# Optimization experiments

Hardware: AMD Instinct MI355X
Metric: run time of the kernel (lower is better)

The kernel has to match this reference:

```python
import jax, jax.numpy as jnp
import numpy as np

EPS = 1e-6


def setup_inputs() -> dict:
    key = jax.random.key(0)
    k1, k2 = jax.random.split(key)
    B, K, N, d = 4, 16, 2048, 256
    return {
        "img_f": jax.random.normal(k1, (B, K, d), dtype=jnp.float32),
        "text_f": jax.random.normal(k2, (N, K, d), dtype=jnp.float32),
        "r": jnp.zeros((4,), dtype=jnp.float32),
        "alp": jnp.array([0.5], dtype=jnp.float32),
        "scale": jnp.array([1.0], dtype=jnp.float32),
        "logits_scales": jnp.array([0.5], dtype=jnp.float32),
    }


def _rc_dist_ItoT(I, T, alpha, beta):
    # I: (B,K,d) images, T: (N,K,d) texts -> dist (B,N)
    B, K, d = I.shape
    lam = (B / d) * jnp.exp(alpha) + EPS
    rho = jnp.exp(beta)
    ItI = jnp.einsum('bkd,bke->bde', I, I)                      # (B,d,d)
    Minv = jnp.linalg.inv(ItI + lam * jnp.eye(d, dtype=I.dtype))
    A = jnp.einsum('bde,bke->bdk', Minv, I)                      # (B,d,K) = Minv @ I^T
    # T_bar[b,n] = I[b] @ A[b] @ T[n]; fuse P = I @ A (B,K,K) to avoid (B,N,d,d) W.
    P = jnp.einsum('bkd,bdj->bkj', I, A)                         # (B,K,K)
    T_bar = jnp.einsum('bkj,njd->bnkd', P, T) * rho              # (B,N,K,d)
    diff = T_bar - T[None]
    return -jnp.sum(diff * diff, axis=-1).mean(axis=-1)          # (B,N)


def _rc_dist_TtoI(I, T, alpha, beta):
    # per-text ridge projector applied to images -> dist (B,N)
    N, K, d = T.shape
    lam = (N / d) * jnp.exp(alpha) + EPS
    rho = jnp.exp(beta)
    TtT = jnp.einsum('nkd,nke->nde', T, T)                       # (N,d,d)
    Minv = jnp.linalg.inv(TtT + lam * jnp.eye(d, dtype=T.dtype))
    A = jnp.einsum('nde,nke->ndk', Minv, T)                      # (N,d,K)
    Q = jnp.einsum('nkd,ndj->nkj', T, A)                         # (N,K,K)
    I_bar = jnp.einsum('nkj,bjd->nbkd', Q, I) * rho              # (N,B,K,d)
    diff = I_bar - I[None]
    return (-jnp.sum(diff * diff, axis=-1).mean(axis=-1)).T      # (B,N)


def reference(img_f, text_f, r, alp, scale, logits_scales):
    d1 = _rc_dist_ItoT(img_f, text_f, r[0], r[1])
    d2 = _rc_dist_TtoI(img_f, text_f, r[2], r[3])
    rc_dist = alp * d1 + (1.0 - alp) * d2
    logits = rc_dist * scale
    logits_pre = jax.nn.log_softmax(logits, axis=1)
    return logits_pre, jax.nn.sigmoid(logits_scales)
```

## Files before the change

kernel.cpp:

```cpp
#include <hip/hip_runtime.h>
#include <math.h>

#define Bq 4
#define Kq 16
#define Nq 2048
#define Dq 256

typedef float f32x4 __attribute__((ext_vector_type(4)));
typedef short s16x8 __attribute__((ext_vector_type(8)));
typedef unsigned int u32;

union frag_u { s16x8 v; u32 w[4]; };


static __device__ __forceinline__ u32 cvtpk(float a, float b) {
    u32 r;
    asm("v_cvt_pk_bf16_f32 %0, %1, %2" : "=v"(r) : "v"(a), "v"(b));
    return r;
}

static __device__ __forceinline__ void cvt2(float a, float b, u32* hw, u32* lw) {
    const u32 h = cvtpk(a, b);
    const float h0 = __uint_as_float(h << 16);
    const float h1 = __uint_as_float(h & 0xFFFF0000u);
    *hw = h;
    *lw = cvtpk(a - h0, b - h1);
}

static __device__ __forceinline__ void conv8(const f32x4 a, const f32x4 b,
                                             s16x8* hi, s16x8* lo) {
    frag_u H, L;
    cvt2(a[0], a[1], &H.w[0], &L.w[0]);
    cvt2(a[2], a[3], &H.w[1], &L.w[1]);
    cvt2(b[0], b[1], &H.w[2], &L.w[2]);
    cvt2(b[2], b[3], &H.w[3], &L.w[3]);
    *hi = H.v; *lo = L.v;
}

static __device__ __forceinline__ float rdlane(float x, int l) {
    return __uint_as_float((u32)__builtin_amdgcn_readlane((int)__float_as_uint(x), l));
}

#define MFMA(A, B, C) __builtin_amdgcn_mfma_f32_16x16x32_bf16((A), (B), (C), 0, 0, 0)

static __device__ __forceinline__ f32x4 gram2(const f32x4* x, f32x4 g) {
    s16x8 hi, lo;
    conv8(x[0], x[1], &hi, &lo);
    g = MFMA(hi, hi, g); g = MFMA(hi, lo, g); g = MFMA(lo, hi, g);
    conv8(x[2], x[3], &hi, &lo);
    g = MFMA(hi, hi, g); g = MFMA(hi, lo, g); g = MFMA(lo, hi, g);
    return g;
}

static __device__ __forceinline__ f32x4 solve_S(f32x4 g, float lam, float rho,
                                                float (*scr)[20], int lane) {
    const int ccol = lane & 15, kgrp = lane >> 4, arow = ccol, j = ccol;
    *reinterpret_cast<f32x4*>(&scr[ccol][kgrp * 4]) = g;
    __builtin_amdgcn_wave_barrier();
    float A[16], rhs[16];
    {
        const float* col = &scr[j][0];
        const f32x4 c0 = *reinterpret_cast<const f32x4*>(col + 0);
        const f32x4 c1 = *reinterpret_cast<const f32x4*>(col + 4);
        const f32x4 c2 = *reinterpret_cast<const f32x4*>(col + 8);
        const f32x4 c3 = *reinterpret_cast<const f32x4*>(col + 12);
        float gv[16];
#pragma unroll
        for (int q = 0; q < 4; ++q) {
            gv[q] = c0[q]; gv[4 + q] = c1[q]; gv[8 + q] = c2[q]; gv[12 + q] = c3[q];
        }
#pragma unroll
        for (int i = 0; i < 16; ++i) {
            const float dv = (i == j) ? lam : 0.f;
            A[i]   = gv[i] + dv;
            rhs[i] = (rho - 1.f) * gv[i] - dv;
        }
    }
    __builtin_amdgcn_wave_barrier();

#pragma unroll
    for (int k = 0; k < Kq; ++k) {
        const float pinv = 1.0f / rdlane(A[k], k);
        A[k]   *= pinv;
        rhs[k] *= pinv;
#pragma unroll
        for (int i = 0; i < 16; ++i) {
            if (i == k) continue;
            const float fac = rdlane(A[i], k);
            A[i]   = fmaf(-fac, A[k],   A[i]);
            rhs[i] = fmaf(-fac, rhs[k], rhs[i]);
        }
    }
#pragma unroll
    for (int i = 0; i < 16; ++i) scr[i][j] = rhs[i];
    __builtin_amdgcn_wave_barrier();

    frag_u H, L;
#pragma unroll
    for (int e = 0; e < 8; e += 2) {
        const int kk = (kgrp & 1) * 8 + e;
        const bool vld = (lane < 32);
        const float m0 = vld ? scr[arow][kk]     : 0.f;
        const float m1 = vld ? scr[arow][kk + 1] : 0.f;
        cvt2(m0, m1, &H.w[e >> 1], &L.w[e >> 1]);
    }
    f32x4 s = {0.f, 0.f, 0.f, 0.f};
    s = MFMA(H.v, H.v, s); s = MFMA(H.v, L.v, s); s = MFMA(L.v, H.v, s);
    return s;
}

__global__ __launch_bounds__(64) void img_kernel(const float* __restrict__ img,
                                                 const float* __restrict__ r,
                                                 float* __restrict__ ws) {
    __shared__ __align__(16) float scr[16][20];
    const int lane = threadIdx.x;
    const int b    = blockIdx.x;
    const int arow = lane & 15, kgrp = lane >> 4;

    const float* base = img + b * (Kq * Dq) + arow * Dq + kgrp * 8;
    f32x4 g = {0.f, 0.f, 0.f, 0.f};
#pragma unroll
    for (int c = 0; c < 8; c += 2) {
        f32x4 x[4];
        x[0] = *reinterpret_cast<const f32x4*>(base + c * 32);
        x[1] = *reinterpret_cast<const f32x4*>(base + c * 32 + 4);
        x[2] = *reinterpret_cast<const f32x4*>(base + (c + 1) * 32);
        x[3] = *reinterpret_cast<const f32x4*>(base + (c + 1) * 32 + 4);
        g = gram2(x, g);
    }
    const float lam = (float(Bq) / float(Dq)) * expf(r[0]) + 1e-6f;
    const float rho = expf(r[1]);
    const f32x4 s = solve_S(g, lam, rho, scr, lane);
    reinterpret_cast<f32x4*>(ws)[b * 64 + lane]        = s;
    reinterpret_cast<f32x4*>(ws + 1024)[b * 64 + lane] = g;
}

__global__ __launch_bounds__(256) void text_kernel(const float* __restrict__ text,
                                                   const float* __restrict__ r,
                                                   const float* __restrict__ alp,
                                                   const float* __restrict__ scale,
                                                   float* __restrict__ ws) {
    __shared__ __align__(16) f32x4 shG[4][64];
    __shared__ __align__(16) float scr[16][20];
    const int tid  = threadIdx.x;
    const int w    = tid >> 6, lane = tid & 63;
    const int arow = lane & 15, kgrp = lane >> 4;
    const int n    = blockIdx.x;

    const float* base = text + n * (Kq * Dq) + arow * Dq + kgrp * 8;
    f32x4 x[4];
    x[0] = *reinterpret_cast<const f32x4*>(base + (2 * w) * 32);
    x[1] = *reinterpret_cast<const f32x4*>(base + (2 * w) * 32 + 4);
    x[2] = *reinterpret_cast<const f32x4*>(base + (2 * w + 1) * 32);
    x[3] = *reinterpret_cast<const f32x4*>(base + (2 * w + 1) * 32 + 4);

    f32x4 g = {0.f, 0.f, 0.f, 0.f};
    g = gram2(x, g);
    shG[w][lane] = g;
    __syncthreads();
    if (w != 0) return;

    const f32x4 gT = shG[0][lane] + shG[1][lane] + shG[2][lane] + shG[3][lane];
    const float lamT = (float(Nq) / float(Dq)) * expf(r[2]) + 1e-6f;
    const float rhoT = expf(r[3]);
    const f32x4 sT = solve_S(gT, lamT, rhoT, scr, lane);

    f32x4 s1v[4], giv[4];
#pragma unroll
    for (int b = 0; b < 4; ++b) {
        s1v[b] = reinterpret_cast<const f32x4*>(ws)[b * 64 + lane];
        giv[b] = reinterpret_cast<const f32x4*>(ws + 1024)[b * 64 + lane];
    }
    float p[8];
#pragma unroll
    for (int b = 0; b < 4; ++b) {
        p[b]     = s1v[b][0] * gT[0] + s1v[b][1] * gT[1] + s1v[b][2] * gT[2] + s1v[b][3] * gT[3];
        p[4 + b] = giv[b][0] * sT[0] + giv[b][1] * sT[1] + giv[b][2] * sT[2] + giv[b][3] * sT[3];
    }
#pragma unroll
    for (int off = 32; off; off >>= 1) {
#pragma unroll
        for (int q = 0; q < 8; ++q) p[q] += __shfl_down(p[q], off, 64);
    }
    if (lane == 0) {
        const float a = alp[0], sc = scale[0];
        float* logits = ws + 2048;
#pragma unroll
        for (int b = 0; b < 4; ++b) {
            const float d1 = -p[b] * (1.f / Kq);
            const float d2 = -p[4 + b] * (1.f / Kq);
            logits[b * Nq + n] = sc * (a * d1 + (1.f - a) * d2);
        }
    }
}

__global__ __launch_bounds__(256) void softmax_kernel(const float* __restrict__ logits,
                                                      const float* __restrict__ lsc,
                                                      float* __restrict__ out) {
    const int b   = blockIdx.x;
    const int tid = threadIdx.x;
    const float* row = logits + b * Nq;
    __shared__ float sh[4];
    float v[8];
    float mx = -INFINITY;
#pragma unroll
    for (int q = 0; q < 8; ++q) {
        v[q] = row[tid + q * 256];
        mx = fmaxf(mx, v[q]);
    }
#pragma unroll
    for (int off = 32; off; off >>= 1) mx = fmaxf(mx, __shfl_down(mx, off, 64));
    if ((tid & 63) == 0) sh[tid >> 6] = mx;
    __syncthreads();
    mx = fmaxf(fmaxf(sh[0], sh[1]), fmaxf(sh[2], sh[3]));

    float sum = 0.f;
#pragma unroll
    for (int q = 0; q < 8; ++q) sum += expf(v[q] - mx);
#pragma unroll
    for (int off = 32; off; off >>= 1) sum += __shfl_down(sum, off, 64);
    __syncthreads();
    if ((tid & 63) == 0) sh[tid >> 6] = sum;
    __syncthreads();
    sum = sh[0] + sh[1] + sh[2] + sh[3];

    const float lse = mx + logf(sum);
#pragma unroll
    for (int q = 0; q < 8; ++q) out[b * Nq + tid + q * 256] = v[q] - lse;
    if (b == 0 && tid == 0) out[Bq * Nq] = 1.f / (1.f + expf(-lsc[0]));
}

extern "C" void kernel_launch(void* const* d_in, const int* in_sizes, int n_in,
                              void* d_out, int out_size, void* d_ws, size_t ws_size,
                              hipStream_t stream) {
    const float* img   = (const float*)d_in[0];
    const float* text  = (const float*)d_in[1];
    const float* r     = (const float*)d_in[2];
    const float* alp   = (const float*)d_in[3];
    const float* scale = (const float*)d_in[4];
    const float* lsc   = (const float*)d_in[5];
    float* ws  = (float*)d_ws;
    float* out = (float*)d_out;

    img_kernel<<<Bq, 64, 0, stream>>>(img, r, ws);
    text_kernel<<<Nq, 256, 0, stream>>>(text, r, alp, scale, ws);
    softmax_kernel<<<Bq, 256, 0, stream>>>(ws + 2048, lsc, out);
}
```

Baseline: 23.07 us.

## Distribute Gauss-Jordan 16x16 solve across all 64 lanes via LDS augmented matrix

Replaces the per-lane register Gauss-Jordan solve, where 16 lanes each held a full column and pivots were fetched with readlane, with an LDS-resident augmented matrix. Each of the 64 lanes updates 4 rows of one column per pivot step. This is meant to use the whole wavefront and cut register pressure, at the cost of LDS round-trips and a rolled loop with wave barriers on every pivot step. It also stops unrolling the image gram loop.

```diff
diff --git a/kernel.cpp b/kernel.cpp
--- a/kernel.cpp
+++ b/kernel.cpp
@@ -37,10 +37,6 @@
     *hi = H.v; *lo = L.v;
 }
 
-static __device__ __forceinline__ float rdlane(float x, int l) {
-    return __uint_as_float((u32)__builtin_amdgcn_readlane((int)__float_as_uint(x), l));
-}
-
 #define MFMA(A, B, C) __builtin_amdgcn_mfma_f32_16x16x32_bf16((A), (B), (C), 0, 0, 0)
 
 static __device__ __forceinline__ f32x4 gram2(const f32x4* x, f32x4 g) {
@@ -52,56 +48,47 @@
     return g;
 }
 
-static __device__ __forceinline__ f32x4 solve_S(f32x4 g, float lam, float rho,
-                                                float (*scr)[20], int lane) {
-    const int ccol = lane & 15, kgrp = lane >> 4, arow = ccol, j = ccol;
-    *reinterpret_cast<f32x4*>(&scr[ccol][kgrp * 4]) = g;
+static __device__ __forceinline__ f32x4 solve_S_lds(f32x4 g, float lam, float rho,
+                                                    float (*Aug)[34], int lane) {
+    const int ccol = lane & 15, kgrp = lane >> 4, arow = ccol;
+#pragma unroll
+    for (int q = 0; q < 4; ++q) {
+        const int rr = kgrp * 4 + q;
+        const float dv = (rr == ccol) ? lam : 0.f;
+        float2 pr; pr.x = g[q] + dv; pr.y = (rho - 1.f) * g[q] - dv;
+        *reinterpret_cast<float2*>(&Aug[rr][2 * ccol]) = pr;
+    }
     __builtin_amdgcn_wave_barrier();
-    float A[16], rhs[16];
-    {
-        const float* col = &scr[j][0];
-        const f32x4 c0 = *reinterpret_cast<const f32x4*>(col + 0);
-        const f32x4 c1 = *reinterpret_cast<const f32x4*>(col + 4);
-        const f32x4 c2 = *reinterpret_cast<const f32x4*>(col + 8);
-        const f32x4 c3 = *reinterpret_cast<const f32x4*>(col + 12);
-        float gv[16];
+
+#pragma unroll 1
+    for (int k = 0; k < Kq; ++k) {
+        const float2 pv = *reinterpret_cast<const float2*>(&Aug[k][2 * k]);
+        const float pinv = 1.f / pv.x;
+        const float2 pk = *reinterpret_cast<const float2*>(&Aug[k][2 * ccol]);
+        float fac[4];
+#pragma unroll
+        for (int q = 0; q < 4; ++q) fac[q] = Aug[kgrp * 4 + q][2 * k];
+        __builtin_amdgcn_wave_barrier();
 #pragma unroll
         for (int q = 0; q < 4; ++q) {
-            gv[q] = c0[q]; gv[4 + q] = c1[q]; gv[8 + q] = c2[q]; gv[12 + q] = c3[q];
+            const int rr = kgrp * 4 + q;
+            float2 cur = *reinterpret_cast<const float2*>(&Aug[rr][2 * ccol]);
+            const float f = fac[q] * pinv;
+            float2 nw;
+            nw.x = (rr == k) ? pk.x * pinv : cur.x - f * pk.x;
+            nw.y = (rr == k) ? pk.y * pinv : cur.y - f * pk.y;
+            *reinterpret_cast<float2*>(&Aug[rr][2 * ccol]) = nw;
         }
-#pragma unroll
-        for (int i = 0; i < 16; ++i) {
-            const float dv = (i == j) ? lam : 0.f;
-            A[i]   = gv[i] + dv;
-            rhs[i] = (rho - 1.f) * gv[i] - dv;
-        }
-    }
-    __builtin_amdgcn_wave_barrier();
-
-#pragma unroll
-    for (int k = 0; k < Kq; ++k) {
-        const float pinv = 1.0f / rdlane(A[k], k);
-        A[k]   *= pinv;
-        rhs[k] *= pinv;
-#pragma unroll
-        for (int i = 0; i < 16; ++i) {
-            if (i == k) continue;
-            const float fac = rdlane(A[i], k);
-            A[i]   = fmaf(-fac, A[k],   A[i]);
-            rhs[i] = fmaf(-fac, rhs[k], rhs[i]);
-        }
-    }
-#pragma unroll
-    for (int i = 0; i < 16; ++i) scr[i][j] = rhs[i];
-    __builtin_amdgcn_wave_barrier();
+        __builtin_amdgcn_wave_barrier();
+    }
 
     frag_u H, L;
 #pragma unroll
     for (int e = 0; e < 8; e += 2) {
         const int kk = (kgrp & 1) * 8 + e;
         const bool vld = (lane < 32);
-        const float m0 = vld ? scr[arow][kk]     : 0.f;
-        const float m1 = vld ? scr[arow][kk + 1] : 0.f;
+        const float m0 = vld ? Aug[arow][2 * kk + 1]       : 0.f;
+        const float m1 = vld ? Aug[arow][2 * (kk + 1) + 1] : 0.f;
         cvt2(m0, m1, &H.w[e >> 1], &L.w[e >> 1]);
     }
     f32x4 s = {0.f, 0.f, 0.f, 0.f};
@@ -112,14 +99,14 @@
 __global__ __launch_bounds__(64) void img_kernel(const float* __restrict__ img,
                                                  const float* __restrict__ r,
                                                  float* __restrict__ ws) {
-    __shared__ __align__(16) float scr[16][20];
+    __shared__ __align__(16) float Aug[Kq][34];
     const int lane = threadIdx.x;
     const int b    = blockIdx.x;
     const int arow = lane & 15, kgrp = lane >> 4;
 
     const float* base = img + b * (Kq * Dq) + arow * Dq + kgrp * 8;
     f32x4 g = {0.f, 0.f, 0.f, 0.f};
-#pragma unroll
+#pragma unroll 1
     for (int c = 0; c < 8; c += 2) {
         f32x4 x[4];
         x[0] = *reinterpret_cast<const f32x4*>(base + c * 32);
@@ -130,7 +117,7 @@
     }
     const float lam = (float(Bq) / float(Dq)) * expf(r[0]) + 1e-6f;
     const float rho = expf(r[1]);
-    const f32x4 s = solve_S(g, lam, rho, scr, lane);
+    const f32x4 s = solve_S_lds(g, lam, rho, Aug, lane);
     reinterpret_cast<f32x4*>(ws)[b * 64 + lane]        = s;
     reinterpret_cast<f32x4*>(ws + 1024)[b * 64 + lane] = g;
 }
@@ -141,7 +128,7 @@
                                                    const float* __restrict__ scale,
                                                    float* __restrict__ ws) {
     __shared__ __align__(16) f32x4 shG[4][64];
-    __shared__ __align__(16) float scr[16][20];
+    __shared__ __align__(16) float Aug[Kq][34];
     const int tid  = threadIdx.x;
     const int w    = tid >> 6, lane = tid & 63;
     const int arow = lane & 15, kgrp = lane >> 4;
@@ -155,15 +142,14 @@
     x[3] = *reinterpret_cast<const f32x4*>(base + (2 * w + 1) * 32 + 4);
 
     f32x4 g = {0.f, 0.f, 0.f, 0.f};
-    g = gram2(x, g);
-    shG[w][lane] = g;
+    shG[w][lane] = gram2(x, g);
     __syncthreads();
     if (w != 0) return;
 
     const f32x4 gT = shG[0][lane] + shG[1][lane] + shG[2][lane] + shG[3][lane];
     const float lamT = (float(Nq) / float(Dq)) * expf(r[2]) + 1e-6f;
     const float rhoT = expf(r[3]);
-    const f32x4 sT = solve_S(gT, lamT, rhoT, scr, lane);
+    const f32x4 sT = solve_S_lds(gT, lamT, rhoT, Aug, lane);
 
     f32x4 s1v[4], giv[4];
 #pragma unroll
```

After: 28.73 us. +24.5%, slower.
